# Kernel optimization log

Hardware: AMD Instinct MI355X
Metric: run time of the kernel (lower is better)

Reference implementation:

```python
import jax, jax.numpy as jnp
import numpy as np
import math

B, MSA, L, D = 1, 64, 256, 512
H = 8
DH = D // H  # 64


def setup_inputs() -> dict:
    key = jax.random.key(0)
    ks = jax.random.split(key, 6)
    x = jax.random.normal(ks[0], (B, MSA, L, D), dtype=jnp.float32)
    Wq = jax.random.normal(ks[1], (D, D), dtype=jnp.float32) * (1.0 / math.sqrt(D))
    Wk = jax.random.normal(ks[2], (D, D), dtype=jnp.float32) * (1.0 / math.sqrt(D))
    Wv = jax.random.normal(ks[3], (D, D), dtype=jnp.float32) * (1.0 / math.sqrt(D))
    aK = jax.random.normal(ks[4], (L, L, DH), dtype=jnp.float32)
    aV = jax.random.normal(ks[5], (L, L, DH), dtype=jnp.float32)
    return {"x": x, "Wq": Wq, "Wk": Wk, "Wv": Wv, "aK": aK, "aV": aV}


def _proj(t, W, b, m, l, h, dh):
    # nn.Linear(bias=False): t @ W.T, then split heads -> (B,H,MSA,L,dh)
    y = jnp.einsum('bmld,ed->bmle', t, W).reshape(b, m, l, h, dh)
    return jnp.transpose(y, (0, 3, 1, 2, 4))


def reference(x, Wq, Wk, Wv, aK, aV):
    b, m, l, d = x.shape
    h, dh = H, DH
    q = _proj(x, Wq, b, m, l, h, dh)  # (B,H,MSA,L,dh)
    k = _proj(x, Wk, b, m, l, h, dh)
    v = _proj(x, Wv, b, m, l, h, dh)
    # content score + relative-position score
    e1 = jnp.einsum('bhmid,bhmjd->bhmij', q, k)           # (B,H,MSA,L,L)
    e2 = jnp.einsum('bhmid,ijd->bhmij', q, aK)            # (B,H,MSA,L,L)
    alpha = jax.nn.softmax((e1 + e2) / math.sqrt(dh), axis=-1)
    z1 = jnp.einsum('bhmij,bhmjd->bhmid', alpha, v)       # content output
    z2 = jnp.einsum('bhmij,ijd->bhmid', alpha, aV)        # relative-V output
    z = (z1 + z2).sum(axis=2)                             # sum over MSA -> (B,H,L,dh)
    out = jnp.transpose(z, (0, 2, 1, 3)).reshape(b, l, d) # (B,L,D)
    return out
```

## Files before the change

kernel.cpp:

```cpp
#include <hip/hip_runtime.h>

#define THREADS 256

typedef unsigned short u16;
typedef __attribute__((ext_vector_type(8))) short bf16x8;
typedef __attribute__((ext_vector_type(4))) float f32x4;

__device__ __forceinline__ u16 f2bf(float f) {
  unsigned int u = __float_as_uint(f);
  u += 0x7fffu + ((u >> 16) & 1u);
  return (u16)(u >> 16);
}
__device__ __forceinline__ float bf2f(u16 s) {
  return __uint_as_float(((unsigned int)s) << 16);
}
__device__ __forceinline__ bf16x8 ld8g(const u16* p) {
  return *reinterpret_cast<const bf16x8*>(p);
}
__device__ __forceinline__ bf16x8 ld8s(const u16* p) {
  return *reinterpret_cast<const bf16x8*>(p);
}
__device__ __forceinline__ void st4bf(u16* dst, float4 v) {
  unsigned int lo = (unsigned int)f2bf(v.x) | ((unsigned int)f2bf(v.y) << 16);
  unsigned int hi = (unsigned int)f2bf(v.z) | ((unsigned int)f2bf(v.w) << 16);
  uint2 u; u.x = lo; u.y = hi;
  *reinterpret_cast<uint2*>(dst) = u;
}
__device__ __forceinline__ uint4 pack8(float4 a, float4 b) {
  uint4 r;
  r.x = (unsigned int)f2bf(a.x) | ((unsigned int)f2bf(a.y) << 16);
  r.y = (unsigned int)f2bf(a.z) | ((unsigned int)f2bf(a.w) << 16);
  r.z = (unsigned int)f2bf(b.x) | ((unsigned int)f2bf(b.y) << 16);
  r.w = (unsigned int)f2bf(b.z) | ((unsigned int)f2bf(b.w) << 16);
  return r;
}
typedef __attribute__((address_space(1))) const unsigned int g_u32;
typedef __attribute__((address_space(3))) unsigned int l_u32;
__device__ __forceinline__ void async16(const u16* g, u16* l) {
  __builtin_amdgcn_global_load_lds((g_u32*)g, (l_u32*)l, 16, 0, 0);
}

__global__ __launch_bounds__(THREADS) void cast_xw(
    const float* __restrict__ x, const float* __restrict__ wq,
    const float* __restrict__ wk, const float* __restrict__ wv,
    u16* __restrict__ xb, u16* __restrict__ wqb, u16* __restrict__ wkb,
    u16* __restrict__ wvb) {
  int t = blockIdx.x * THREADS + threadIdx.x;
  if (t < 2097152) {
    st4bf(xb + t * 4, reinterpret_cast<const float4*>(x)[t]);
  } else if (t < 2162688) {
    int q = t - 2097152;
    st4bf(wqb + q * 4, reinterpret_cast<const float4*>(wq)[q]);
  } else if (t < 2228224) {
    int q = t - 2162688;
    st4bf(wkb + q * 4, reinterpret_cast<const float4*>(wk)[q]);
  } else if (t < 2293760) {
    int q = t - 2228224;
    st4bf(wvb + q * 4, reinterpret_cast<const float4*>(wv)[q]);
  }
}

__global__ __launch_bounds__(THREADS) void proj_gemm(
    const u16* __restrict__ xb, const u16* __restrict__ wb,
    u16* __restrict__ qh, u16* __restrict__ kb, u16* __restrict__ vt) {
  const int bm = blockIdx.x / 12, bn = blockIdx.x % 12;
  const int tid = threadIdx.x;
  const int wave = tid >> 6, lane = tid & 63;
  const int quad = lane >> 4, l15 = lane & 15;
  __shared__ __align__(16) u16 smem[9216];
  u16* At = smem;
  u16* Bt = smem + 4096;

  const int rowL = lane >> 2;
  const int chunkL = (lane & 3) ^ ((lane >> 3) & 3);
  const u16* gA = xb + (size_t)(bm * 128 + wave * 32 + rowL) * 512 + chunkL * 8;
  const u16* gB = wb + (size_t)(bn * 128 + wave * 32 + rowL) * 512 + chunkL * 8;
  u16* lA = At + wave * 1024;
  u16* lB = Bt + wave * 1024;

  const int rw0 = (wave & 1) * 64, cw0 = (wave >> 1) * 64;
  const int swz = (quad ^ ((l15 >> 1) & 3)) * 8;

  f32x4 acc[4][4];
#pragma unroll
  for (int mt = 0; mt < 4; ++mt)
#pragma unroll
    for (int nt = 0; nt < 4; ++nt) acc[mt][nt] = (f32x4){0.f, 0.f, 0.f, 0.f};

  for (int s = 0; s < 16; ++s) {
    __syncthreads();
    async16(gA + s * 32, lA);
    async16(gA + s * 32 + 8192, lA + 512);
    async16(gB + s * 32, lB);
    async16(gB + s * 32 + 8192, lB + 512);
    __syncthreads();
    bf16x8 af[4], bf[4];
#pragma unroll
    for (int mt = 0; mt < 4; ++mt)
      af[mt] = ld8s(At + (rw0 + mt * 16 + l15) * 32 + swz);
#pragma unroll
    for (int nt = 0; nt < 4; ++nt)
      bf[nt] = ld8s(Bt + (cw0 + nt * 16 + l15) * 32 + swz);
#pragma unroll
    for (int mt = 0; mt < 4; ++mt)
#pragma unroll
      for (int nt = 0; nt < 4; ++nt)
        acc[mt][nt] = __builtin_amdgcn_mfma_f32_16x16x32_bf16(af[mt], bf[nt], acc[mt][nt], 0, 0, 0);
  }

  const int mat = bn >> 2;
  const int h0 = (bn & 3) * 2;
  const int m = bm >> 1;
  const int l0 = (bm & 1) * 128;

  if (mat < 2) {
    u16* dstb = (mat == 0) ? qh : kb;
    const int il = tid >> 1, cc = (tid & 1) * 32;
#pragma unroll
    for (int p = 0; p < 2; ++p) {
      __syncthreads();
      if ((wave >> 1) == p) {
#pragma unroll
        for (int mt = 0; mt < 4; ++mt)
#pragma unroll
          for (int nt = 0; nt < 4; ++nt)
#pragma unroll
            for (int r = 0; r < 4; ++r)
              smem[(rw0 + mt * 16 + quad * 4 + r) * 72 + nt * 16 + l15] =
                  f2bf(acc[mt][nt][r]);
      }
      __syncthreads();
      u16* dst = dstb + ((size_t)((h0 + p) * 64 + m) * 256 + l0 + il) * 64 + cc;
      uint4 v0 = *reinterpret_cast<uint4*>(&smem[il * 72 + cc]);
      uint4 v1 = *reinterpret_cast<uint4*>(&smem[il * 72 + cc + 8]);
      uint4 v2 = *reinterpret_cast<uint4*>(&smem[il * 72 + cc + 16]);
      uint4 v3 = *reinterpret_cast<uint4*>(&smem[il * 72 + cc + 24]);
      *reinterpret_cast<uint4*>(dst) = v0;
      *reinterpret_cast<uint4*>(dst + 8) = v1;
      *reinterpret_cast<uint4*>(dst + 16) = v2;
      *reinterpret_cast<uint4*>(dst + 24) = v3;
    }
  } else {
    const int tl = tid >> 2, cc = (tid & 3) * 32;
#pragma unroll
    for (int p = 0; p < 2; ++p) {
      __syncthreads();
      if ((wave >> 1) == p) {
#pragma unroll
        for (int mt = 0; mt < 4; ++mt)
#pragma unroll
          for (int nt = 0; nt < 4; ++nt)
#pragma unroll
            for (int r = 0; r < 4; ++r)
              smem[(nt * 16 + l15) * 136 + rw0 + mt * 16 + quad * 4 + r] =
                  f2bf(acc[mt][nt][r]);
      }
      __syncthreads();
      int hm = (h0 + p) * 64 + m;
      u16* dst = vt + (size_t)hm * 16384 + tl * 256 + l0 + cc;
      uint4 v0 = *reinterpret_cast<uint4*>(&smem[tl * 136 + cc]);
      uint4 v1 = *reinterpret_cast<uint4*>(&smem[tl * 136 + cc + 8]);
      uint4 v2 = *reinterpret_cast<uint4*>(&smem[tl * 136 + cc + 16]);
      uint4 v3 = *reinterpret_cast<uint4*>(&smem[tl * 136 + cc + 24]);
      *reinterpret_cast<uint4*>(dst) = v0;
      *reinterpret_cast<uint4*>(dst + 8) = v1;
      *reinterpret_cast<uint4*>(dst + 16) = v2;
      *reinterpret_cast<uint4*>(dst + 24) = v3;
    }
  }
}

__global__ __launch_bounds__(THREADS) void e2_k(
    const u16* __restrict__ qh, const float* __restrict__ aK,
    u16* __restrict__ e2g) {
  const int i = blockIdx.x >> 3, hmt = blockIdx.x & 7;
  const int tid = threadIdx.x;
  const int wave = tid >> 6, lane = tid & 63;
  const int quad = lane >> 4, l15 = lane & 15;
  __shared__ u16 aKl[256 * 72];
#pragma unroll
  for (int c = 0; c < 8; ++c) {
    int fidx = c * 2048 + tid * 8;
    int j = fidx >> 6, d = fidx & 63;
    float4 f0 = *reinterpret_cast<const float4*>(aK + i * 16384 + fidx);
    float4 f1 = *reinterpret_cast<const float4*>(aK + i * 16384 + fidx + 4);
    *reinterpret_cast<uint4*>(&aKl[j * 72 + d]) = pack8(f0, f1);
  }
  __syncthreads();
  f32x4 acc[16];
#pragma unroll
  for (int nt = 0; nt < 16; ++nt) acc[nt] = (f32x4){0.f, 0.f, 0.f, 0.f};
  bf16x8 a[2];
#pragma unroll
  for (int ks = 0; ks < 2; ++ks)
    a[ks] = ld8g(qh + ((hmt * 64 + wave * 16 + l15) * 256 + i) * 64 + ks * 32 + quad * 8);
#pragma unroll
  for (int nt = 0; nt < 16; ++nt) {
#pragma unroll
    for (int ks = 0; ks < 2; ++ks) {
      bf16x8 b = ld8s(&aKl[(nt * 16 + l15) * 72 + ks * 32 + quad * 8]);
      acc[nt] = __builtin_amdgcn_mfma_f32_16x16x32_bf16(a[ks], b, acc[nt], 0, 0, 0);
    }
  }
  __syncthreads();
  u16* S = aKl;
#pragma unroll
  for (int nt = 0; nt < 16; ++nt)
#pragma unroll
    for (int r = 0; r < 4; ++r)
      S[(wave * 16 + quad * 4 + r) * 264 + nt * 16 + l15] = f2bf(acc[nt][r]);
  __syncthreads();
#pragma unroll
  for (int c = 0; c < 8; ++c) {
    int lin = c * 2048 + tid * 8;
    int row = lin >> 8, col = lin & 255;
    uint4 v = *reinterpret_cast<uint4*>(&S[row * 264 + col]);
    *reinterpret_cast<uint4*>(e2g + ((size_t)(hmt * 64 + row) * 256 + i) * 256 + col) = v;
  }
}

__global__ __launch_bounds__(THREADS) void attn_k(
    const u16* __restrict__ qh, const u16* __restrict__ kb,
    const u16* __restrict__ vt, u16* __restrict__ e2g,
    u16* __restrict__ z1p) {
  const int bi = blockIdx.x;
  const int hm = bi & 511, it = bi >> 9;
  const int tid = threadIdx.x;
  const int wave = tid >> 6, lane = tid & 63;
  const int quad = lane >> 4, l15 = lane & 15;
  __shared__ u16 As[4 * 4224];
  u16* W = &As[wave * 4224];
#pragma unroll
  for (int c = 0; c < 8; ++c) {
    int lin = c * 512 + lane * 8;
    int row = lin >> 8, col = lin & 255;
    uint4 v = *reinterpret_cast<const uint4*>(
        e2g + ((size_t)hm * 256 + it * 64 + wave * 16 + row) * 256 + col);
    *reinterpret_cast<uint4*>(&W[row * 264 + col]) = v;
  }
  __syncthreads();
  f32x4 acc[16];
#pragma unroll
  for (int nt = 0; nt < 16; ++nt) acc[nt] = (f32x4){0.f, 0.f, 0.f, 0.f};
  bf16x8 a[2];
#pragma unroll
  for (int ks = 0; ks < 2; ++ks)
    a[ks] = ld8g(qh + ((size_t)hm * 256 + it * 64 + wave * 16 + l15) * 64 + ks * 32 + quad * 8);
#pragma unroll
  for (int nt = 0; nt < 16; ++nt) {
#pragma unroll
    for (int ks = 0; ks < 2; ++ks) {
      bf16x8 b = ld8g(kb + ((size_t)hm * 256 + nt * 16 + l15) * 64 + ks * 32 + quad * 8);
      acc[nt] = __builtin_amdgcn_mfma_f32_16x16x32_bf16(a[ks], b, acc[nt], 0, 0, 0);
    }
  }
#pragma unroll
  for (int nt = 0; nt < 16; ++nt) {
#pragma unroll
    for (int r = 0; r < 4; ++r) {
      float e2v = bf2f(W[(quad * 4 + r) * 264 + nt * 16 + l15]);
      acc[nt][r] = (acc[nt][r] + e2v) * 0.125f;
    }
  }
#pragma unroll
  for (int r = 0; r < 4; ++r) {
    float mx = -3.0e38f;
#pragma unroll
    for (int nt = 0; nt < 16; ++nt) mx = fmaxf(mx, acc[nt][r]);
    for (int msk = 1; msk < 16; msk <<= 1) mx = fmaxf(mx, __shfl_xor(mx, msk));
    float s = 0.f;
#pragma unroll
    for (int nt = 0; nt < 16; ++nt) {
      float p = expf(acc[nt][r] - mx);
      acc[nt][r] = p;
      s += p;
    }
    for (int msk = 1; msk < 16; msk <<= 1) s += __shfl_xor(s, msk);
    float inv = 1.0f / s;
    int lrow = quad * 4 + r;
#pragma unroll
    for (int nt = 0; nt < 16; ++nt)
      W[lrow * 264 + nt * 16 + l15] = f2bf(acc[nt][r] * inv);
  }
  __syncthreads();
#pragma unroll
  for (int c = 0; c < 8; ++c) {
    int lin = c * 512 + lane * 8;
    int row = lin >> 8, col = lin & 255;
    uint4 v = *reinterpret_cast<uint4*>(&W[row * 264 + col]);
    *reinterpret_cast<uint4*>(
        e2g + ((size_t)hm * 256 + it * 64 + wave * 16 + row) * 256 + col) = v;
  }
  f32x4 acc2[4];
#pragma unroll
  for (int nt = 0; nt < 4; ++nt) acc2[nt] = (f32x4){0.f, 0.f, 0.f, 0.f};
#pragma unroll
  for (int ks = 0; ks < 8; ++ks) {
    bf16x8 a2 = ld8s(&W[l15 * 264 + ks * 32 + quad * 8]);
#pragma unroll
    for (int nt = 0; nt < 4; ++nt) {
      bf16x8 b2 = ld8g(vt + (size_t)hm * 16384 + (nt * 16 + l15) * 256 + ks * 32 + quad * 8);
      acc2[nt] = __builtin_amdgcn_mfma_f32_16x16x32_bf16(a2, b2, acc2[nt], 0, 0, 0);
    }
  }
  __syncthreads();
#pragma unroll
  for (int nt = 0; nt < 4; ++nt)
#pragma unroll
    for (int r = 0; r < 4; ++r)
      W[(quad * 4 + r) * 264 + nt * 16 + l15] = f2bf(acc2[nt][r]);
  __syncthreads();
  {
    int row = lane >> 2, col = (lane & 3) * 16;
    uint4 v0 = *reinterpret_cast<uint4*>(&W[row * 264 + col]);
    uint4 v1 = *reinterpret_cast<uint4*>(&W[row * 264 + col + 8]);
    u16* dst = z1p + (size_t)hm * 16384 + (it * 64 + wave * 16 + row) * 64 + col;
    *reinterpret_cast<uint4*>(dst) = v0;
    *reinterpret_cast<uint4*>(dst + 8) = v1;
  }
}

__global__ __launch_bounds__(THREADS) void beta_k(
    const u16* __restrict__ alphag, float* __restrict__ beta) {
  const int b = blockIdx.x;
  const int h = b >> 8, i = b & 255;
  const int j = threadIdx.x;
  float s = 0.f;
  const u16* base = alphag + (size_t)(h * 64) * 65536 + i * 256 + j;
#pragma unroll 4
  for (int m = 0; m < 64; ++m) s += bf2f(base[(size_t)m * 65536]);
  beta[(h * 256 + i) * 256 + j] = s;
}

__global__ __launch_bounds__(THREADS) void z2_k(
    const float* __restrict__ beta, const float* __restrict__ aV,
    float* __restrict__ z2b) {
  const int i = blockIdx.x;
  const int tid = threadIdx.x;
  const int wave = tid >> 6, lane = tid & 63;
  const int quad = lane >> 4, l15 = lane & 15;
  __shared__ u16 aVl[64 * 264];
#pragma unroll
  for (int c = 0; c < 8; ++c) {
    int fidx = c * 2048 + tid * 8;
    int j = fidx >> 6, d = fidx & 63;
    float4 f0 = *reinterpret_cast<const float4*>(aV + (size_t)i * 16384 + fidx);
    float4 f1 = *reinterpret_cast<const float4*>(aV + (size_t)i * 16384 + fidx + 4);
    float fv[8] = {f0.x, f0.y, f0.z, f0.w, f1.x, f1.y, f1.z, f1.w};
#pragma unroll
    for (int u = 0; u < 8; ++u) aVl[(d + u) * 264 + j] = f2bf(fv[u]);
  }
  __syncthreads();
  f32x4 acc = (f32x4){0.f, 0.f, 0.f, 0.f};
#pragma unroll
  for (int ks = 0; ks < 8; ++ks) {
    u16 ab[8];
    if (l15 < 8) {
      const float* bp = beta + (l15 * 256 + i) * 256 + ks * 32 + quad * 8;
      float4 f0 = *reinterpret_cast<const float4*>(bp);
      float4 f1 = *reinterpret_cast<const float4*>(bp + 4);
      ab[0] = f2bf(f0.x); ab[1] = f2bf(f0.y); ab[2] = f2bf(f0.z); ab[3] = f2bf(f0.w);
      ab[4] = f2bf(f1.x); ab[5] = f2bf(f1.y); ab[6] = f2bf(f1.z); ab[7] = f2bf(f1.w);
    } else {
#pragma unroll
      for (int u = 0; u < 8; ++u) ab[u] = 0;
    }
    bf16x8 a = *reinterpret_cast<bf16x8*>(ab);
    bf16x8 b = ld8s(&aVl[(wave * 16 + l15) * 264 + ks * 32 + quad * 8]);
    acc = __builtin_amdgcn_mfma_f32_16x16x32_bf16(a, b, acc, 0, 0, 0);
  }
#pragma unroll
  for (int r = 0; r < 4; ++r) {
    int h = quad * 4 + r;
    if (h < 8) z2b[i * 512 + h * 64 + wave * 16 + l15] = acc[r];
  }
}

__global__ __launch_bounds__(THREADS) void reduce_k(
    const u16* __restrict__ z1p, const float* __restrict__ z2b,
    float* __restrict__ out) {
  int o = blockIdx.x * THREADS + threadIdx.x;
  int i = o >> 9, e = o & 511;
  int h = e >> 6, d = e & 63;
  float s = z2b[o];
  const u16* base = z1p + (size_t)(h * 64) * 16384 + i * 64 + d;
#pragma unroll 4
  for (int m = 0; m < 64; ++m) s += bf2f(base[(size_t)m * 16384]);
  out[o] = s;
}

extern "C" void kernel_launch(void* const* d_in, const int* in_sizes, int n_in,
                              void* d_out, int out_size, void* d_ws, size_t ws_size,
                              hipStream_t stream) {
  const float* x  = (const float*)d_in[0];
  const float* wq = (const float*)d_in[1];
  const float* wk = (const float*)d_in[2];
  const float* wv = (const float*)d_in[3];
  const float* aK = (const float*)d_in[4];
  const float* aV = (const float*)d_in[5];
  float* out = (float*)d_out;

  char* ws = (char*)d_ws;
  u16* xb    = (u16*)(ws + 0);
  u16* wqb   = (u16*)(ws + 16777216);
  u16* wkb   = (u16*)(ws + 17301504);
  u16* wvb   = (u16*)(ws + 17825792);
  float* beta= (float*)(ws + 18350080);
  float* z2b = (float*)(ws + 20447232);
  u16* qh    = (u16*)(ws + 35127296);
  u16* kb    = (u16*)(ws + 51904512);
  u16* vt    = (u16*)(ws + 68681728);
  u16* e2g   = (u16*)(ws + 85458944);
  u16* z1p   = xb;

  cast_xw<<<8960, THREADS, 0, stream>>>(x, wq, wk, wv, xb, wqb, wkb, wvb);
  proj_gemm<<<1536, THREADS, 0, stream>>>(xb, wqb, qh, kb, vt);
  e2_k<<<2048, THREADS, 0, stream>>>(qh, aK, e2g);
  attn_k<<<2048, THREADS, 0, stream>>>(qh, kb, vt, e2g, z1p);
  beta_k<<<2048, THREADS, 0, stream>>>(e2g, beta);
  z2_k<<<256, THREADS, 0, stream>>>(beta, aV, z2b);
  reduce_k<<<512, THREADS, 0, stream>>>(z1p, z2b, out);
}
```

Baseline: 300.3 us.

## Store e2/alpha in MFMA-fragment order to skip LDS staging and barriers

Changes the global e2/alpha buffer to a layout that matches the MFMA accumulator fragment, so e2_k writes straight from registers and attn_k reads e2 into registers and writes alpha back with no LDS round trip or block barriers. beta_k is rewritten to read this layout with vector loads over fewer blocks, and reduce_k is vectorised to 8 outputs per thread. The aim is to cut LDS traffic, barriers and uncoalesced 2-byte loads. It also swaps expf for __expf, which is less precise. attn_k still reuses the per-wave LDS region without the removed barriers, which is safe only because each wave uses its own slice.

```diff
diff --git a/kernel.cpp b/kernel.cpp
--- a/kernel.cpp
+++ b/kernel.cpp
@@ -39,6 +39,7 @@
 __device__ __forceinline__ void async16(const u16* g, u16* l) {
   __builtin_amdgcn_global_load_lds((g_u32*)g, (l_u32*)l, 16, 0, 0);
 }
+
 
 __global__ __launch_bounds__(THREADS) void cast_xw(
     const float* __restrict__ x, const float* __restrict__ wq,
@@ -172,7 +173,7 @@
 
 __global__ __launch_bounds__(THREADS) void e2_k(
     const u16* __restrict__ qh, const float* __restrict__ aK,
-    u16* __restrict__ e2g) {
+    u16* __restrict__ e2c) {
   const int i = blockIdx.x >> 3, hmt = blockIdx.x & 7;
   const int tid = threadIdx.x;
   const int wave = tid >> 6, lane = tid & 63;
@@ -182,8 +183,8 @@
   for (int c = 0; c < 8; ++c) {
     int fidx = c * 2048 + tid * 8;
     int j = fidx >> 6, d = fidx & 63;
-    float4 f0 = *reinterpret_cast<const float4*>(aK + i * 16384 + fidx);
-    float4 f1 = *reinterpret_cast<const float4*>(aK + i * 16384 + fidx + 4);
+    float4 f0 = *reinterpret_cast<const float4*>(aK + (size_t)i * 16384 + fidx);
+    float4 f1 = *reinterpret_cast<const float4*>(aK + (size_t)i * 16384 + fidx + 4);
     *reinterpret_cast<uint4*>(&aKl[j * 72 + d]) = pack8(f0, f1);
   }
   __syncthreads();
@@ -193,7 +194,7 @@
   bf16x8 a[2];
 #pragma unroll
   for (int ks = 0; ks < 2; ++ks)
-    a[ks] = ld8g(qh + ((hmt * 64 + wave * 16 + l15) * 256 + i) * 64 + ks * 32 + quad * 8);
+    a[ks] = ld8g(qh + ((size_t)(hmt * 64 + wave * 16 + l15) * 256 + i) * 64 + ks * 32 + quad * 8);
 #pragma unroll
   for (int nt = 0; nt < 16; ++nt) {
 #pragma unroll
@@ -202,26 +203,23 @@
       acc[nt] = __builtin_amdgcn_mfma_f32_16x16x32_bf16(a[ks], b, acc[nt], 0, 0, 0);
     }
   }
-  __syncthreads();
-  u16* S = aKl;
-#pragma unroll
-  for (int nt = 0; nt < 16; ++nt)
-#pragma unroll
-    for (int r = 0; r < 4; ++r)
-      S[(wave * 16 + quad * 4 + r) * 264 + nt * 16 + l15] = f2bf(acc[nt][r]);
-  __syncthreads();
-#pragma unroll
-  for (int c = 0; c < 8; ++c) {
-    int lin = c * 2048 + tid * 8;
-    int row = lin >> 8, col = lin & 255;
-    uint4 v = *reinterpret_cast<uint4*>(&S[row * 264 + col]);
-    *reinterpret_cast<uint4*>(e2g + ((size_t)(hmt * 64 + row) * 256 + i) * 256 + col) = v;
+  const int it = i >> 6, wt = (i >> 4) & 3, qt = (i >> 2) & 3, rt = i & 3;
+  u16* ebase = e2c + (size_t)(qt * 16 + l15) * 64 + rt * 16;
+#pragma unroll
+  for (int re = 0; re < 4; ++re) {
+    int hm = hmt * 64 + wave * 16 + quad * 4 + re;
+    u16 buf[16];
+#pragma unroll
+    for (int nt = 0; nt < 16; ++nt) buf[nt] = f2bf(acc[nt][re]);
+    u16* d = ebase + ((size_t)(hm * 4 + it) * 4 + wt) * 4096;
+    reinterpret_cast<uint4*>(d)[0] = reinterpret_cast<uint4*>(buf)[0];
+    reinterpret_cast<uint4*>(d)[1] = reinterpret_cast<uint4*>(buf)[1];
   }
 }
 
 __global__ __launch_bounds__(THREADS) void attn_k(
     const u16* __restrict__ qh, const u16* __restrict__ kb,
-    const u16* __restrict__ vt, u16* __restrict__ e2g,
+    const u16* __restrict__ vt, u16* __restrict__ e2c,
     u16* __restrict__ z1p) {
   const int bi = blockIdx.x;
   const int hm = bi & 511, it = bi >> 9;
@@ -230,15 +228,13 @@
   const int quad = lane >> 4, l15 = lane & 15;
   __shared__ u16 As[4 * 4224];
   u16* W = &As[wave * 4224];
-#pragma unroll
-  for (int c = 0; c < 8; ++c) {
-    int lin = c * 512 + lane * 8;
-    int row = lin >> 8, col = lin & 255;
-    uint4 v = *reinterpret_cast<const uint4*>(
-        e2g + ((size_t)hm * 256 + it * 64 + wave * 16 + row) * 256 + col);
-    *reinterpret_cast<uint4*>(&W[row * 264 + col]) = v;
-  }
-  __syncthreads();
+
+  u16* eb = e2c + (((size_t)hm * 4 + it) * 4 + wave) * 4096 + (size_t)lane * 64;
+  uint4 e2v[8];
+#pragma unroll
+  for (int c = 0; c < 8; ++c) e2v[c] = reinterpret_cast<const uint4*>(eb)[c];
+  const u16* e2a = reinterpret_cast<const u16*>(e2v);
+
   f32x4 acc[16];
 #pragma unroll
   for (int nt = 0; nt < 16; ++nt) acc[nt] = (f32x4){0.f, 0.f, 0.f, 0.f};
@@ -255,13 +251,12 @@
     }
   }
 #pragma unroll
-  for (int nt = 0; nt < 16; ++nt) {
-#pragma unroll
-    for (int r = 0; r < 4; ++r) {
-      float e2v = bf2f(W[(quad * 4 + r) * 264 + nt * 16 + l15]);
-      acc[nt][r] = (acc[nt][r] + e2v) * 0.125f;
-    }
-  }
+  for (int nt = 0; nt < 16; ++nt)
+#pragma unroll
+    for (int r = 0; r < 4; ++r)
+      acc[nt][r] = (acc[nt][r] + bf2f(e2a[r * 16 + nt])) * 0.125f;
+
+  u16 a16[64];
 #pragma unroll
   for (int r = 0; r < 4; ++r) {
     float mx = -3.0e38f;
@@ -271,7 +266,7 @@
     float s = 0.f;
 #pragma unroll
     for (int nt = 0; nt < 16; ++nt) {
-      float p = expf(acc[nt][r] - mx);
+      float p = __expf(acc[nt][r] - mx);
       acc[nt][r] = p;
       s += p;
     }
@@ -279,18 +274,16 @@
     float inv = 1.0f / s;
     int lrow = quad * 4 + r;
 #pragma unroll
-    for (int nt = 0; nt < 16; ++nt)
-      W[lrow * 264 + nt * 16 + l15] = f2bf(acc[nt][r] * inv);
-  }
-  __syncthreads();
-#pragma unroll
-  for (int c = 0; c < 8; ++c) {
-    int lin = c * 512 + lane * 8;
-    int row = lin >> 8, col = lin & 255;
-    uint4 v = *reinterpret_cast<uint4*>(&W[row * 264 + col]);
-    *reinterpret_cast<uint4*>(
-        e2g + ((size_t)hm * 256 + it * 64 + wave * 16 + row) * 256 + col) = v;
-  }
+    for (int nt = 0; nt < 16; ++nt) {
+      u16 pb = f2bf(acc[nt][r] * inv);
+      a16[r * 16 + nt] = pb;
+      W[lrow * 264 + nt * 16 + l15] = pb;
+    }
+  }
+#pragma unroll
+  for (int c = 0; c < 8; ++c)
+    reinterpret_cast<uint4*>(eb)[c] = reinterpret_cast<const uint4*>(a16)[c];
+
   f32x4 acc2[4];
 #pragma unroll
   for (int nt = 0; nt < 4; ++nt) acc2[nt] = (f32x4){0.f, 0.f, 0.f, 0.f};
@@ -303,13 +296,11 @@
       acc2[nt] = __builtin_amdgcn_mfma_f32_16x16x32_bf16(a2, b2, acc2[nt], 0, 0, 0);
     }
   }
-  __syncthreads();
 #pragma unroll
   for (int nt = 0; nt < 4; ++nt)
 #pragma unroll
     for (int r = 0; r < 4; ++r)
       W[(quad * 4 + r) * 264 + nt * 16 + l15] = f2bf(acc2[nt][r]);
-  __syncthreads();
   {
     int row = lane >> 2, col = (lane & 3) * 16;
     uint4 v0 = *reinterpret_cast<uint4*>(&W[row * 264 + col]);
@@ -321,15 +312,26 @@
 }
 
 __global__ __launch_bounds__(THREADS) void beta_k(
-    const u16* __restrict__ alphag, float* __restrict__ beta) {
+    const u16* __restrict__ alphac, float* __restrict__ beta) {
   const int b = blockIdx.x;
-  const int h = b >> 8, i = b & 255;
-  const int j = threadIdx.x;
-  float s = 0.f;
-  const u16* base = alphag + (size_t)(h * 64) * 65536 + i * 256 + j;
-#pragma unroll 4
-  for (int m = 0; m < 64; ++m) s += bf2f(base[(size_t)m * 65536]);
-  beta[(h * 256 + i) * 256 + j] = s;
+  const int h = b >> 6, it = (b >> 4) & 3, wt = (b >> 2) & 3, qt = b & 3;
+  const int tid = threadIdx.x;
+  const int l15 = tid >> 4, sub = tid & 15, r = sub >> 2, ntq = sub & 3;
+  const u16* base = alphac + ((size_t)((h * 64) * 4 + it) * 4 + wt) * 4096 +
+                    (size_t)(qt * 16 + l15) * 64 + r * 16 + ntq * 4;
+  float s0 = 0.f, s1 = 0.f, s2 = 0.f, s3 = 0.f;
+#pragma unroll 8
+  for (int m = 0; m < 64; ++m) {
+    uint2 v = *reinterpret_cast<const uint2*>(base + (size_t)m * 65536);
+    const u16* p = reinterpret_cast<const u16*>(&v);
+    s0 += bf2f(p[0]); s1 += bf2f(p[1]); s2 += bf2f(p[2]); s3 += bf2f(p[3]);
+  }
+  const int i = it * 64 + wt * 16 + qt * 4 + r;
+  float* o = beta + ((size_t)h * 256 + i) * 256 + l15;
+  o[(ntq * 4 + 0) * 16] = s0;
+  o[(ntq * 4 + 1) * 16] = s1;
+  o[(ntq * 4 + 2) * 16] = s2;
+  o[(ntq * 4 + 3) * 16] = s3;
 }
 
 __global__ __launch_bounds__(THREADS) void z2_k(
@@ -356,7 +358,7 @@
   for (int ks = 0; ks < 8; ++ks) {
     u16 ab[8];
     if (l15 < 8) {
-      const float* bp = beta + (l15 * 256 + i) * 256 + ks * 32 + quad * 8;
+      const float* bp = beta + ((size_t)l15 * 256 + i) * 256 + ks * 32 + quad * 8;
       float4 f0 = *reinterpret_cast<const float4*>(bp);
       float4 f1 = *reinterpret_cast<const float4*>(bp + 4);
       ab[0] = f2bf(f0.x); ab[1] = f2bf(f0.y); ab[2] = f2bf(f0.z); ab[3] = f2bf(f0.w);
@@ -372,21 +374,31 @@
 #pragma unroll
   for (int r = 0; r < 4; ++r) {
     int h = quad * 4 + r;
-    if (h < 8) z2b[i * 512 + h * 64 + wave * 16 + l15] = acc[r];
+    if (h < 8) z2b[(size_t)i * 512 + h * 64 + wave * 16 + l15] = acc[r];
   }
 }
 
 __global__ __launch_bounds__(THREADS) void reduce_k(
     const u16* __restrict__ z1p, const float* __restrict__ z2b,
     float* __restrict__ out) {
-  int o = blockIdx.x * THREADS + threadIdx.x;
-  int i = o >> 9, e = o & 511;
-  int h = e >> 6, d = e & 63;
-  float s = z2b[o];
-  const u16* base = z1p + (size_t)(h * 64) * 16384 + i * 64 + d;
+  int t = blockIdx.x * THREADS + threadIdx.x;
+  size_t o8 = (size_t)t * 8;
+  int i = (int)(o8 >> 9), e0 = (int)(o8 & 511);
+  int h = e0 >> 6, d0 = e0 & 63;
+  float4 s0 = reinterpret_cast<const float4*>(z2b + o8)[0];
+  float4 s1 = reinterpret_cast<const float4*>(z2b + o8)[1];
+  float s[8] = {s0.x, s0.y, s0.z, s0.w, s1.x, s1.y, s1.z, s1.w};
+  const u16* zb = z1p + (size_t)h * 64 * 16384 + (size_t)i * 64 + d0;
 #pragma unroll 4
-  for (int m = 0; m < 64; ++m) s += bf2f(base[(size_t)m * 16384]);
-  out[o] = s;
+  for (int m = 0; m < 64; ++m) {
+    uint4 v = *reinterpret_cast<const uint4*>(zb + (size_t)m * 16384);
+    const u16* p = reinterpret_cast<const u16*>(&v);
+#pragma unroll
+    for (int k = 0; k < 8; ++k) s[k] += bf2f(p[k]);
+  }
+  float4 r0 = {s[0], s[1], s[2], s[3]}, r1 = {s[4], s[5], s[6], s[7]};
+  reinterpret_cast<float4*>(out + o8)[0] = r0;
+  reinterpret_cast<float4*>(out + o8)[1] = r1;
 }
 
 extern "C" void kernel_launch(void* const* d_in, const int* in_sizes, int n_in,
@@ -410,14 +422,14 @@
   u16* qh    = (u16*)(ws + 35127296);
   u16* kb    = (u16*)(ws + 51904512);
   u16* vt    = (u16*)(ws + 68681728);
-  u16* e2g   = (u16*)(ws + 85458944);
+  u16* e2c   = (u16*)(ws + 85458944);
   u16* z1p   = xb;
 
   cast_xw<<<8960, THREADS, 0, stream>>>(x, wq, wk, wv, xb, wqb, wkb, wvb);
   proj_gemm<<<1536, THREADS, 0, stream>>>(xb, wqb, qh, kb, vt);
-  e2_k<<<2048, THREADS, 0, stream>>>(qh, aK, e2g);
-  attn_k<<<2048, THREADS, 0, stream>>>(qh, kb, vt, e2g, z1p);
-  beta_k<<<2048, THREADS, 0, stream>>>(e2g, beta);
+  e2_k<<<2048, THREADS, 0, stream>>>(qh, aK, e2c);
+  attn_k<<<2048, THREADS, 0, stream>>>(qh, kb, vt, e2c, z1p);
+  beta_k<<<512, THREADS, 0, stream>>>(e2c, beta);
   z2_k<<<256, THREADS, 0, stream>>>(beta, aV, z2b);
-  reduce_k<<<512, THREADS, 0, stream>>>(z1p, z2b, out);
-}
+  reduce_k<<<64, THREADS, 0, stream>>>(z1p, z2b, out);
+}
```

Result: slower. 309.6 us (+3.1%).
